# Kernel optimization log

Measured on AMD Instinct MI355X. Metric: run time of the kernel, lower is better.

## Reference

```python
import jax, jax.numpy as jnp
import numpy as np

# Instant-NGP HashGrid constants (match tcnn encoding_config defaults in the module)
N_LEVELS = 16
N_FEATS = 2
LOG2_T = 16
T = 1 << LOG2_T            # hashmap entries per level
BASE_RES = 16
PER_LEVEL_SCALE = 1.5
N_POINTS = 1 << 20
PRIMES = (1, 2654435761, 805459861)  # tcnn spatial-hash primes

# 8 corner offsets of the unit cube, [8,3]
_CORNERS = np.array([[i, j, k] for i in (0, 1) for j in (0, 1) for k in (0, 1)], dtype=np.float32)


def setup_inputs() -> dict:
    key = jax.random.key(0)
    k1, k2 = jax.random.split(key)
    x = jax.random.uniform(k1, (N_POINTS, 3), dtype=jnp.float32)
    # tcnn initializes hash tables uniform in [-1e-4, 1e-4]
    table = jax.random.uniform(k2, (N_LEVELS, T, N_FEATS), minval=-1e-4, maxval=1e-4, dtype=jnp.float32)
    return {"x": x, "table": table}


def _corner_index(grid, res, dense):
    # grid: [N,8,3] int32 corner coordinates -> [N,8] table index
    if dense:
        g = jnp.clip(grid, 0, res - 1)
        return g[..., 0] + g[..., 1] * res + g[..., 2] * res * res
    g = grid.astype(jnp.uint32)
    h = (g[..., 0] * jnp.uint32(PRIMES[0])
         ^ g[..., 1] * jnp.uint32(PRIMES[1])
         ^ g[..., 2] * jnp.uint32(PRIMES[2]))
    return (h & jnp.uint32(T - 1)).astype(jnp.int32)


def _hashgrid_forward(x, table):
    x = x.astype(jnp.float32)
    offs = jnp.asarray(_CORNERS)                      # [8,3]
    outs = []
    for level in range(N_LEVELS):
        # tcnn: grid_scale = base * s^level - 1 ; resolution = ceil(scale)+1
        scale = float(BASE_RES * (PER_LEVEL_SCALE ** level) - 1.0)
        res = int(np.ceil(scale)) + 1
        dense = res ** 3 <= T                          # tcnn uses dense indexing when the grid fits
        pos = x * scale + 0.5                          # [N,3]
        g0 = jnp.floor(pos)
        frac = pos - g0                                # [N,3] trilinear fractions
        grid = (g0[:, None, :] + offs[None]).astype(jnp.int32)   # [N,8,3]
        idx = _corner_index(grid, res, dense)          # [N,8]
        feat = table[level][idx]                       # [N,8,F] irregular gather
        # trilinear weights: prod over dims of frac or (1-frac) per corner
        w = jnp.prod(jnp.where(offs[None] > 0, frac[:, None, :], 1.0 - frac[:, None, :]), axis=-1)  # [N,8]
        outs.append(jnp.sum(w[..., None] * feat, axis=1))        # [N,F]
    return jnp.concatenate(outs, axis=-1)              # [N, L*F] = [N,32]


def reference(x, table):
    return _hashgrid_forward(x, table)
```

## Files before the change

### kernel.cpp

```cpp
#include <hip/hip_runtime.h>
#include <stdint.h>


#define NLVL 16
#define TS 65536
#define P2 2654435761u
#define P3 805459861u

__device__ __forceinline__ float2 f4lo(float4 v) { return make_float2(v.x, v.y); }
__device__ __forceinline__ float2 f4hi(float4 v) { return make_float2(v.z, v.w); }

__global__ __launch_bounds__(256) void hashgrid_fwd(
    const float* __restrict__ x,
    const float* __restrict__ table,
    float* __restrict__ out,
    int n)
{
    const int tid0 = blockIdx.x * 256 + threadIdx.x;
    const int tid = min(tid0, n - 1);

    const float px = x[3 * tid + 0];
    const float py = x[3 * tid + 1];
    const float pz = x[3 * tid + 2];

    const float SCALES[NLVL] = {
        15.0f, 23.0f, 35.0f, 53.0f, 80.0f, 120.5f, 181.25f, 272.375f,
        409.0625f, 614.09375f, 921.640625f, 1382.9609375f,
        2074.94140625f, 3112.912109375f, 4669.8681640625f, 7005.30224609375f};
    const int RESO[NLVL] = {16, 24, 36, 54, 81, 122, 183, 274,
                            411, 616, 923, 1384, 2076, 3114, 4671, 7007};

    float acc[32];

#pragma unroll
    for (int l = 0; l < NLVL; ++l) {
        const float scale = SCALES[l];
        const float fx = px * scale + 0.5f;
        const float fy = py * scale + 0.5f;
        const float fz = pz * scale + 0.5f;
        const float gx = floorf(fx), gy = floorf(fy), gz = floorf(fz);
        const float wx = fx - gx, wy = fy - gy, wz = fz - gz;
        const int ix = (int)gx, iy = (int)gy, iz = (int)gz;

        const float2* tbl = ((const float2*)table) + (size_t)l * TS;

        float2 c0, c1, c2, c3, c4, c5, c6, c7;
        if (l < 3) {
            const int R = RESO[l];
            const int x0 = min(ix, R - 1);
            const int y0 = min(iy, R - 1), y1 = min(iy + 1, R - 1);
            const int z0 = min(iz, R - 1), z1 = min(iz + 1, R - 1);
            const int xb = min(x0, R - 2);
            const bool hi0 = (x0 != xb);
            const int y0R = y0 * R, y1R = y1 * R;
            const int z0R = z0 * R * R, z1R = z1 * R * R;
            const float4 f00 = *(const float4*)(tbl + (xb + y0R + z0R));
            const float4 f01 = *(const float4*)(tbl + (xb + y0R + z1R));
            const float4 f10 = *(const float4*)(tbl + (xb + y1R + z0R));
            const float4 f11 = *(const float4*)(tbl + (xb + y1R + z1R));
            c0 = hi0 ? f4hi(f00) : f4lo(f00);  c4 = f4hi(f00);
            c1 = hi0 ? f4hi(f01) : f4lo(f01);  c5 = f4hi(f01);
            c2 = hi0 ? f4hi(f10) : f4lo(f10);  c6 = f4hi(f10);
            c3 = hi0 ? f4hi(f11) : f4lo(f11);  c7 = f4hi(f11);
        } else {
            const uint32_t bx = (uint32_t)ix;
            const uint32_t hy0 = (uint32_t)iy * P2, hy1 = hy0 + P2;
            const uint32_t hz0 = (uint32_t)iz * P3, hz1 = hz0 + P3;
            const uint32_t b00 = hy0 ^ hz0, b01 = hy0 ^ hz1;
            const uint32_t b10 = hy1 ^ hz0, b11 = hy1 ^ hz1;
            const uint32_t i00 = (bx ^ b00) & (TS - 1);
            const uint32_t i01 = (bx ^ b01) & (TS - 1);
            const uint32_t i10 = (bx ^ b10) & (TS - 1);
            const uint32_t i11 = (bx ^ b11) & (TS - 1);
            const float4* tbl4 = (const float4*)tbl;
            const float4 f00 = tbl4[i00 >> 1];
            const float4 f01 = tbl4[i01 >> 1];
            const float4 f10 = tbl4[i10 >> 1];
            const float4 f11 = tbl4[i11 >> 1];
            c0 = (i00 & 1) ? f4hi(f00) : f4lo(f00);
            c1 = (i01 & 1) ? f4hi(f01) : f4lo(f01);
            c2 = (i10 & 1) ? f4hi(f10) : f4lo(f10);
            c3 = (i11 & 1) ? f4hi(f11) : f4lo(f11);
            if ((ix & 1) == 0) {
                c4 = (i00 & 1) ? f4lo(f00) : f4hi(f00);
                c5 = (i01 & 1) ? f4lo(f01) : f4hi(f01);
                c6 = (i10 & 1) ? f4lo(f10) : f4hi(f10);
                c7 = (i11 & 1) ? f4lo(f11) : f4hi(f11);
            } else {
                const uint32_t bx1 = bx + 1;
                c4 = tbl[(bx1 ^ b00) & (TS - 1)];
                c5 = tbl[(bx1 ^ b01) & (TS - 1)];
                c6 = tbl[(bx1 ^ b10) & (TS - 1)];
                c7 = tbl[(bx1 ^ b11) & (TS - 1)];
            }
        }

        const float ux = 1.0f - wx, uy = 1.0f - wy, uz = 1.0f - wz;
        const float w0 = ux * uy * uz;
        const float w1 = ux * uy * wz;
        const float w2 = ux * wy * uz;
        const float w3 = ux * wy * wz;
        const float w4 = wx * uy * uz;
        const float w5 = wx * uy * wz;
        const float w6 = wx * wy * uz;
        const float w7 = wx * wy * wz;

        acc[2 * l + 0] = w0 * c0.x + w1 * c1.x + w2 * c2.x + w3 * c3.x +
                         w4 * c4.x + w5 * c5.x + w6 * c6.x + w7 * c7.x;
        acc[2 * l + 1] = w0 * c0.y + w1 * c1.y + w2 * c2.y + w3 * c3.y +
                         w4 * c4.y + w5 * c5.y + w6 * c6.y + w7 * c7.y;
    }

    __shared__ float lds[128 * 33];
    const int half = threadIdx.x >> 7;
    const int tl = threadIdx.x & 127;
    float* outb = out + (size_t)blockIdx.x * (256 * 32);
    const long long lim = (long long)n * 32 - (long long)blockIdx.x * (256 * 32);

#pragma unroll
    for (int pass = 0; pass < 2; ++pass) {
        if (half == pass) {
#pragma unroll
            for (int j = 0; j < 32; ++j) lds[tl * 33 + j] = acc[j];
        }
        __syncthreads();
        float* o = outb + pass * (128 * 32);
        const long long plim = lim - pass * (128 * 32);
#pragma unroll
        for (int r = 0; r < 16; ++r) {
            const int g = r * 256 + threadIdx.x;
            const int p = g >> 5, f = g & 31;
            if (g < plim) o[g] = lds[p * 33 + f];
        }
        __syncthreads();
    }
}

extern "C" void kernel_launch(void* const* d_in, const int* in_sizes, int n_in,
                              void* d_out, int out_size, void* d_ws, size_t ws_size,
                              hipStream_t stream) {
    const float* x = (const float*)d_in[0];
    const float* table = (const float*)d_in[1];
    float* out = (float*)d_out;
    const int n = in_sizes[0] / 3;
    const int block = 256;
    const int grid = (n + block - 1) / block;
    hashgrid_fwd<<<grid, block, 0, stream>>>(x, table, out, n);
}
```

Before: 569.0 us.

## Stream per-level results to swizzled LDS and cap registers for occupancy

Result: faster. 528.2 us (-7.2%).

```diff
diff --git a/kernel.cpp b/kernel.cpp
--- a/kernel.cpp
+++ b/kernel.cpp
@@ -7,45 +7,52 @@
 #define P2 2654435761u
 #define P3 805459861u
 
+__constant__ float C_SCALES[NLVL] = {
+    15.0f, 23.0f, 35.0f, 53.0f, 80.0f, 120.5f, 181.25f, 272.375f,
+    409.0625f, 614.09375f, 921.640625f, 1382.9609375f,
+    2074.94140625f, 3112.912109375f, 4669.8681640625f, 7005.30224609375f};
+
 __device__ __forceinline__ float2 f4lo(float4 v) { return make_float2(v.x, v.y); }
 __device__ __forceinline__ float2 f4hi(float4 v) { return make_float2(v.z, v.w); }
 
-__global__ __launch_bounds__(256) void hashgrid_fwd(
+__device__ __forceinline__ void lds_put2(float* s_out, int p, int f2,
+                                         float a, float b) {
+    const int sw = p & 31;
+    const int base = p * 32 + (f2 ^ (sw & 30));
+    if (sw & 1) { s_out[base] = b; s_out[base + 1] = a; }
+    else        { s_out[base] = a; s_out[base + 1] = b; }
+}
+
+__global__ __launch_bounds__(256, 5) void hashgrid_fwd(
     const float* __restrict__ x,
     const float* __restrict__ table,
     float* __restrict__ out,
     int n)
 {
+    __shared__ float s_out[256 * 32];
+
     const int tid0 = blockIdx.x * 256 + threadIdx.x;
     const int tid = min(tid0, n - 1);
+    const int p = threadIdx.x;
 
     const float px = x[3 * tid + 0];
     const float py = x[3 * tid + 1];
     const float pz = x[3 * tid + 2];
 
-    const float SCALES[NLVL] = {
-        15.0f, 23.0f, 35.0f, 53.0f, 80.0f, 120.5f, 181.25f, 272.375f,
-        409.0625f, 614.09375f, 921.640625f, 1382.9609375f,
-        2074.94140625f, 3112.912109375f, 4669.8681640625f, 7005.30224609375f};
-    const int RESO[NLVL] = {16, 24, 36, 54, 81, 122, 183, 274,
-                            411, 616, 923, 1384, 2076, 3114, 4671, 7007};
+    {
+        const int RESO[3] = {16, 24, 36};
+        const float DSC[3] = {15.0f, 23.0f, 35.0f};
+#pragma unroll
+        for (int l = 0; l < 3; ++l) {
+            const float scale = DSC[l];
+            const float fx = px * scale + 0.5f;
+            const float fy = py * scale + 0.5f;
+            const float fz = pz * scale + 0.5f;
+            const float gx = floorf(fx), gy = floorf(fy), gz = floorf(fz);
+            const float wx = fx - gx, wy = fy - gy, wz = fz - gz;
+            const int ix = (int)gx, iy = (int)gy, iz = (int)gz;
 
-    float acc[32];
-
-#pragma unroll
-    for (int l = 0; l < NLVL; ++l) {
-        const float scale = SCALES[l];
-        const float fx = px * scale + 0.5f;
-        const float fy = py * scale + 0.5f;
-        const float fz = pz * scale + 0.5f;
-        const float gx = floorf(fx), gy = floorf(fy), gz = floorf(fz);
-        const float wx = fx - gx, wy = fy - gy, wz = fz - gz;
-        const int ix = (int)gx, iy = (int)gy, iz = (int)gz;
-
-        const float2* tbl = ((const float2*)table) + (size_t)l * TS;
-
-        float2 c0, c1, c2, c3, c4, c5, c6, c7;
-        if (l < 3) {
+            const float2* tbl = ((const float2*)table) + (size_t)l * TS;
             const int R = RESO[l];
             const int x0 = min(ix, R - 1);
             const int y0 = min(iy, R - 1), y1 = min(iy + 1, R - 1);
@@ -58,81 +65,92 @@
             const float4 f01 = *(const float4*)(tbl + (xb + y0R + z1R));
             const float4 f10 = *(const float4*)(tbl + (xb + y1R + z0R));
             const float4 f11 = *(const float4*)(tbl + (xb + y1R + z1R));
-            c0 = hi0 ? f4hi(f00) : f4lo(f00);  c4 = f4hi(f00);
-            c1 = hi0 ? f4hi(f01) : f4lo(f01);  c5 = f4hi(f01);
-            c2 = hi0 ? f4hi(f10) : f4lo(f10);  c6 = f4hi(f10);
-            c3 = hi0 ? f4hi(f11) : f4lo(f11);  c7 = f4hi(f11);
+            const float2 c0 = hi0 ? f4hi(f00) : f4lo(f00), c4 = f4hi(f00);
+            const float2 c1 = hi0 ? f4hi(f01) : f4lo(f01), c5 = f4hi(f01);
+            const float2 c2 = hi0 ? f4hi(f10) : f4lo(f10), c6 = f4hi(f10);
+            const float2 c3 = hi0 ? f4hi(f11) : f4lo(f11), c7 = f4hi(f11);
+
+            const float ux = 1.0f - wx, uy = 1.0f - wy, uz = 1.0f - wz;
+            const float w0 = ux * uy * uz, w1 = ux * uy * wz;
+            const float w2 = ux * wy * uz, w3 = ux * wy * wz;
+            const float w4 = wx * uy * uz, w5 = wx * uy * wz;
+            const float w6 = wx * wy * uz, w7 = wx * wy * wz;
+
+            const float o0 = w0 * c0.x + w1 * c1.x + w2 * c2.x + w3 * c3.x +
+                             w4 * c4.x + w5 * c5.x + w6 * c6.x + w7 * c7.x;
+            const float o1 = w0 * c0.y + w1 * c1.y + w2 * c2.y + w3 * c3.y +
+                             w4 * c4.y + w5 * c5.y + w6 * c6.y + w7 * c7.y;
+            lds_put2(s_out, p, 2 * l, o0, o1);
+        }
+    }
+
+#pragma unroll 2
+    for (int l = 3; l < NLVL; ++l) {
+        const float scale = C_SCALES[l];
+        const float fx = px * scale + 0.5f;
+        const float fy = py * scale + 0.5f;
+        const float fz = pz * scale + 0.5f;
+        const float gx = floorf(fx), gy = floorf(fy), gz = floorf(fz);
+        const float wx = fx - gx, wy = fy - gy, wz = fz - gz;
+        const int ix = (int)gx, iy = (int)gy, iz = (int)gz;
+
+        const float2* tbl = ((const float2*)table) + (size_t)l * TS;
+
+        const uint32_t bx = (uint32_t)ix;
+        const uint32_t hy0 = (uint32_t)iy * P2, hy1 = hy0 + P2;
+        const uint32_t hz0 = (uint32_t)iz * P3, hz1 = hz0 + P3;
+        const uint32_t b00 = hy0 ^ hz0, b01 = hy0 ^ hz1;
+        const uint32_t b10 = hy1 ^ hz0, b11 = hy1 ^ hz1;
+        const uint32_t i00 = (bx ^ b00) & (TS - 1);
+        const uint32_t i01 = (bx ^ b01) & (TS - 1);
+        const uint32_t i10 = (bx ^ b10) & (TS - 1);
+        const uint32_t i11 = (bx ^ b11) & (TS - 1);
+        const float4* tbl4 = (const float4*)tbl;
+        const float4 f00 = tbl4[i00 >> 1];
+        const float4 f01 = tbl4[i01 >> 1];
+        const float4 f10 = tbl4[i10 >> 1];
+        const float4 f11 = tbl4[i11 >> 1];
+        const float2 c0 = (i00 & 1) ? f4hi(f00) : f4lo(f00);
+        const float2 c1 = (i01 & 1) ? f4hi(f01) : f4lo(f01);
+        const float2 c2 = (i10 & 1) ? f4hi(f10) : f4lo(f10);
+        const float2 c3 = (i11 & 1) ? f4hi(f11) : f4lo(f11);
+        float2 c4, c5, c6, c7;
+        if ((ix & 1) == 0) {
+            c4 = (i00 & 1) ? f4lo(f00) : f4hi(f00);
+            c5 = (i01 & 1) ? f4lo(f01) : f4hi(f01);
+            c6 = (i10 & 1) ? f4lo(f10) : f4hi(f10);
+            c7 = (i11 & 1) ? f4lo(f11) : f4hi(f11);
         } else {
-            const uint32_t bx = (uint32_t)ix;
-            const uint32_t hy0 = (uint32_t)iy * P2, hy1 = hy0 + P2;
-            const uint32_t hz0 = (uint32_t)iz * P3, hz1 = hz0 + P3;
-            const uint32_t b00 = hy0 ^ hz0, b01 = hy0 ^ hz1;
-            const uint32_t b10 = hy1 ^ hz0, b11 = hy1 ^ hz1;
-            const uint32_t i00 = (bx ^ b00) & (TS - 1);
-            const uint32_t i01 = (bx ^ b01) & (TS - 1);
-            const uint32_t i10 = (bx ^ b10) & (TS - 1);
-            const uint32_t i11 = (bx ^ b11) & (TS - 1);
-            const float4* tbl4 = (const float4*)tbl;
-            const float4 f00 = tbl4[i00 >> 1];
-            const float4 f01 = tbl4[i01 >> 1];
-            const float4 f10 = tbl4[i10 >> 1];
-            const float4 f11 = tbl4[i11 >> 1];
-            c0 = (i00 & 1) ? f4hi(f00) : f4lo(f00);
-            c1 = (i01 & 1) ? f4hi(f01) : f4lo(f01);
-            c2 = (i10 & 1) ? f4hi(f10) : f4lo(f10);
-            c3 = (i11 & 1) ? f4hi(f11) : f4lo(f11);
-            if ((ix & 1) == 0) {
-                c4 = (i00 & 1) ? f4lo(f00) : f4hi(f00);
-                c5 = (i01 & 1) ? f4lo(f01) : f4hi(f01);
-                c6 = (i10 & 1) ? f4lo(f10) : f4hi(f10);
-                c7 = (i11 & 1) ? f4lo(f11) : f4hi(f11);
-            } else {
-                const uint32_t bx1 = bx + 1;
-                c4 = tbl[(bx1 ^ b00) & (TS - 1)];
-                c5 = tbl[(bx1 ^ b01) & (TS - 1)];
-                c6 = tbl[(bx1 ^ b10) & (TS - 1)];
-                c7 = tbl[(bx1 ^ b11) & (TS - 1)];
-            }
+            const uint32_t bx1 = bx + 1;
+            c4 = tbl[(bx1 ^ b00) & (TS - 1)];
+            c5 = tbl[(bx1 ^ b01) & (TS - 1)];
+            c6 = tbl[(bx1 ^ b10) & (TS - 1)];
+            c7 = tbl[(bx1 ^ b11) & (TS - 1)];
         }
 
         const float ux = 1.0f - wx, uy = 1.0f - wy, uz = 1.0f - wz;
-        const float w0 = ux * uy * uz;
-        const float w1 = ux * uy * wz;
-        const float w2 = ux * wy * uz;
-        const float w3 = ux * wy * wz;
-        const float w4 = wx * uy * uz;
-        const float w5 = wx * uy * wz;
-        const float w6 = wx * wy * uz;
-        const float w7 = wx * wy * wz;
+        const float w0 = ux * uy * uz, w1 = ux * uy * wz;
+        const float w2 = ux * wy * uz, w3 = ux * wy * wz;
+        const float w4 = wx * uy * uz, w5 = wx * uy * wz;
+        const float w6 = wx * wy * uz, w7 = wx * wy * wz;
 
-        acc[2 * l + 0] = w0 * c0.x + w1 * c1.x + w2 * c2.x + w3 * c3.x +
+        const float o0 = w0 * c0.x + w1 * c1.x + w2 * c2.x + w3 * c3.x +
                          w4 * c4.x + w5 * c5.x + w6 * c6.x + w7 * c7.x;
-        acc[2 * l + 1] = w0 * c0.y + w1 * c1.y + w2 * c2.y + w3 * c3.y +
+        const float o1 = w0 * c0.y + w1 * c1.y + w2 * c2.y + w3 * c3.y +
                          w4 * c4.y + w5 * c5.y + w6 * c6.y + w7 * c7.y;
+        lds_put2(s_out, p, 2 * l, o0, o1);
     }
 
-    __shared__ float lds[128 * 33];
-    const int half = threadIdx.x >> 7;
-    const int tl = threadIdx.x & 127;
+    __syncthreads();
+
     float* outb = out + (size_t)blockIdx.x * (256 * 32);
     const long long lim = (long long)n * 32 - (long long)blockIdx.x * (256 * 32);
-
 #pragma unroll
-    for (int pass = 0; pass < 2; ++pass) {
-        if (half == pass) {
-#pragma unroll
-            for (int j = 0; j < 32; ++j) lds[tl * 33 + j] = acc[j];
-        }
-        __syncthreads();
-        float* o = outb + pass * (128 * 32);
-        const long long plim = lim - pass * (128 * 32);
-#pragma unroll
-        for (int r = 0; r < 16; ++r) {
-            const int g = r * 256 + threadIdx.x;
-            const int p = g >> 5, f = g & 31;
-            if (g < plim) o[g] = lds[p * 33 + f];
-        }
-        __syncthreads();
+    for (int r = 0; r < 32; ++r) {
+        const int g = r * 256 + threadIdx.x;
+        const int pp = g >> 5, f = g & 31;
+        const float v = s_out[pp * 32 + (f ^ (pp & 31))];
+        if (g < lim) outb[g] = v;
     }
 }
 
```
